# Kernel tuning notes

Hardware: AMD Instinct MI355X
Metric: run time of the kernel (lower is better)

The kernel has to match this reference:

```python
import jax, jax.numpy as jnp
import numpy as np

C = 192  # in_channels
B, S, L = 4, 64, 512  # batch, spatial (patch pixels), seq_len (num patches)


def setup_inputs() -> dict:
    key = jax.random.key(0)
    ks = jax.random.split(key, 6)
    scale_in = 1.0 / np.sqrt(C)
    return {
        "query": jax.random.normal(ks[0], (B, C, S, L), jnp.float32),
        "key": jax.random.normal(ks[1], (B, C, S, L), jnp.float32),
        "value": jax.random.normal(ks[2], (B, C, S, L), jnp.float32),
        "in_proj_weight": jax.random.normal(ks[3], (1 + 2 * C, C, 1, 1), jnp.float32) * scale_in,
        "in_proj_bias": jnp.zeros((1 + 2 * C,), jnp.float32),
        "out_proj_weight": jax.random.normal(ks[4], (C, C, 1, 1), jnp.float32) * scale_in,
        "out_proj_bias": jnp.zeros((C,), jnp.float32),
    }


def reference(query, key, value, in_proj_weight, in_proj_bias, out_proj_weight, out_proj_bias):
    # Separable (linear) attention, MobileViTv2-style.
    c = query.shape[1]
    w = in_proj_weight[:, :, 0, 0]           # (1+2C, C)
    wq, wk, wv = w[:1], w[1:1 + c], w[1 + c:]
    bq, bk, bv = in_proj_bias[:1], in_proj_bias[1:1 + c], in_proj_bias[1 + c:]

    # 1x1 conv projections (pointwise GEMMs over channels)
    q = jnp.einsum('oc,bcsl->bosl', wq, query) + bq[None, :, None, None]   # (B,1,S,L)
    k = jnp.einsum('oc,bcsl->bosl', wk, key) + bk[None, :, None, None]     # (B,C,S,L)
    v = jnp.einsum('oc,bcsl->bosl', wv, value) + bv[None, :, None, None]   # (B,C,S,L)

    # Context scores: softmax over token axis (seq_len); dropout_p=0 (eval)
    context_scores = jax.nn.softmax(q, axis=-1)                            # (B,1,S,L)

    # Weighted context pooling over tokens -> global context per spatial pixel
    context = jnp.sum(k * context_scores, axis=-1, keepdims=True)          # (B,C,S,1)

    # Broadcast multiply with gated value
    out = jax.nn.relu(v) * context                                         # (B,C,S,L)

    # Out projection (1x1 conv)
    wo = out_proj_weight[:, :, 0, 0]
    out = jnp.einsum('oc,bcsl->bosl', wo, out) + out_proj_bias[None, :, None, None]
    return out
```

## Files before the change

kernel.cpp:

```cpp
#include <hip/hip_runtime.h>

#define B_ 4
#define C_ 192
#define S_ 64
#define L_ 512

typedef _Float16 h8 __attribute__((ext_vector_type(8)));
typedef _Float16 h4 __attribute__((ext_vector_type(4)));
typedef _Float16 h2 __attribute__((ext_vector_type(2)));
typedef float f4 __attribute__((ext_vector_type(4)));

__device__ __forceinline__ int swz_l(int l) { return ((l >> 2) ^ l) & 7; }

__global__ __launch_bounds__(512) void k_prep(
    const float* __restrict__ W, const float* __restrict__ Bi,
    const float* __restrict__ Wo, const float* __restrict__ Bo,
    _Float16* __restrict__ wvh, _Float16* __restrict__ woh,
    float* __restrict__ bvf, float* __restrict__ bof,
    float* __restrict__ wkT)
{
    int n = blockIdx.x * 512 + threadIdx.x;
    if (n < 36864)       wvh[n] = (_Float16)W[37056 + n];
    else if (n < 73728)  woh[n - 36864] = (_Float16)Wo[n - 36864];
    else if (n < 73920)  bvf[n - 73728] = Bi[1 + C_ + (n - 73728)];
    else if (n < 74112)  bof[n - 73920] = Bo[n - 73920];
    else if (n < 110976) {
        int m = n - 74112;
        int c = m / C_, o = m - c * C_;
        wkT[m] = W[(1 + o) * C_ + c];
    }
}

__global__ __launch_bounds__(1024) void kA_front(
    const float* __restrict__ Q, const float* __restrict__ K,
    const float* __restrict__ W, const float* __restrict__ Bi,
    const float* __restrict__ wkT, float* __restrict__ ctxb)
{
    __shared__ __attribute__((aligned(16))) float sm_part[8 * 512];
    __shared__ float sm_p[512];
    __shared__ float sm_kbar[C_];
    __shared__ float sm_red[8];
    __shared__ float sm_red2[8];

    const int t = threadIdx.x;
    const int b = blockIdx.x >> 6, s = blockIdx.x & 63;
    const int lane = t & 63, w = t >> 6;

    {
        const int qid = t & 127;
        const int cg  = t >> 7;
        const float* qp = Q + (((size_t)b * C_ + cg * 24) * S_ + s) * L_ + qid * 4;
        f4 a; a[0] = 0.f; a[1] = 0.f; a[2] = 0.f; a[3] = 0.f;
#pragma unroll 8
        for (int c = 0; c < 24; ++c) {
            float wq = W[cg * 24 + c];
            f4 x = *(const f4*)(qp + (size_t)c * (S_ * L_));
            a[0] += wq * x[0]; a[1] += wq * x[1]; a[2] += wq * x[2]; a[3] += wq * x[3];
        }
        *(f4*)&sm_part[cg * 512 + qid * 4] = a;
    }
    __syncthreads();

    float q = 0.f, e = 0.f;
    if (t < 512) {
        q = ((sm_part[t] + sm_part[512 + t]) + (sm_part[1024 + t] + sm_part[1536 + t]))
          + ((sm_part[2048 + t] + sm_part[2560 + t]) + (sm_part[3072 + t] + sm_part[3584 + t]));
        float m = q;
#pragma unroll
        for (int off = 32; off >= 1; off >>= 1) m = fmaxf(m, __shfl_down(m, off));
        if (lane == 0) sm_red[w] = m;
    }
    __syncthreads();
    if (t < 512) {
        float bm = sm_red[0];
#pragma unroll
        for (int i = 1; i < 8; ++i) bm = fmaxf(bm, sm_red[i]);
        e = __expf(q - bm);
        float sum = e;
#pragma unroll
        for (int off = 32; off >= 1; off >>= 1) sum += __shfl_down(sum, off);
        if (lane == 0) sm_red2[w] = sum;
    }
    __syncthreads();
    if (t < 512) {
        float tot = 0.f;
#pragma unroll
        for (int i = 0; i < 8; ++i) tot += sm_red2[i];
        sm_p[t] = e / tot;
    }
    __syncthreads();

    {
        const f4* pp = (const f4*)sm_p;
        f4 p0 = pp[lane], p1 = pp[lane + 64];
#pragma unroll 4
        for (int r = 0; r < 12; ++r) {
            int c = w * 12 + r;
            const f4* kp = (const f4*)(K + (((size_t)b * C_ + c) * S_ + s) * L_);
            f4 x0 = kp[lane], x1 = kp[lane + 64];
            float d = x0[0]*p0[0] + x0[1]*p0[1] + x0[2]*p0[2] + x0[3]*p0[3]
                    + x1[0]*p1[0] + x1[1]*p1[1] + x1[2]*p1[2] + x1[3]*p1[3];
#pragma unroll
            for (int off = 32; off >= 1; off >>= 1) d += __shfl_down(d, off);
            if (lane == 0) sm_kbar[c] = d;
        }
    }
    __syncthreads();

    if (t < C_) {
        float a0 = 0.f, a1 = 0.f, a2 = 0.f, a3 = 0.f;
        for (int c = 0; c < C_; c += 4) {
            a0 += wkT[(c + 0) * C_ + t] * sm_kbar[c + 0];
            a1 += wkT[(c + 1) * C_ + t] * sm_kbar[c + 1];
            a2 += wkT[(c + 2) * C_ + t] * sm_kbar[c + 2];
            a3 += wkT[(c + 3) * C_ + t] * sm_kbar[c + 3];
        }
        ctxb[(size_t)blockIdx.x * C_ + t] = (a0 + a1) + (a2 + a3) + Bi[1 + t];
    }
}

__global__ __launch_bounds__(512, 4) void k_main(
    const float* __restrict__ V,
    const _Float16* __restrict__ wvh,
    const _Float16* __restrict__ woh,
    const float* __restrict__ ctxb,
    const float* __restrict__ bvf,
    const float* __restrict__ bof,
    float* __restrict__ Out)
{
    __shared__ __attribute__((aligned(16))) _Float16 sm_v[64 * 192];
    __shared__ __attribute__((aligned(16))) _Float16 sm_u[64 * 192];

    const int t = threadIdx.x;
    const int bs = blockIdx.x >> 3;
    const int chunk = blockIdx.x & 7;
    const int b = bs >> 6, s = bs & 63;
    const int l0 = chunk * 64;
    const int w = t >> 6, lane = t & 63;
    const int quad = lane >> 4, n16 = lane & 15;

    const int oB = (w & 3) * 48;
    const int lB = (w >> 2) * 32;

    {
        const int tx = t & 15, rp = t >> 4;
        h2* smv2 = (h2*)sm_v;
#pragma unroll
        for (int i = 0; i < 3; ++i) {
            int cp = i * 32 + rp;
            const float* vp = V + ((size_t)(b * C_ + 2 * cp) * S_ + s) * L_ + l0 + tx * 4;
            f4 x0 = *(const f4*)vp;
            f4 x1 = *(const f4*)(vp + S_ * L_);
#pragma unroll
            for (int k = 0; k < 4; ++k) {
                int l = tx * 4 + k;
                int dw = l * 96 + (((cp >> 2) ^ swz_l(l)) << 2) + (cp & 3);
                h2 hh; hh[0] = (_Float16)x0[k]; hh[1] = (_Float16)x1[k];
                smv2[dw] = hh;
            }
        }
    }

    h8 wv_fr[6][3];
#pragma unroll
    for (int kt = 0; kt < 6; ++kt)
#pragma unroll
        for (int i = 0; i < 3; ++i)
            wv_fr[kt][i] = *(const h8*)(wvh + (size_t)(oB + i * 16 + n16) * C_ + kt * 32 + quad * 8);

    __syncthreads();

    f4 acc[3][2];
#pragma unroll
    for (int i = 0; i < 3; ++i)
#pragma unroll
        for (int j = 0; j < 2; ++j) acc[i][j] = (f4)0.f;

#pragma unroll
    for (int kt = 0; kt < 6; ++kt) {
        h8 bfr[2];
#pragma unroll
        for (int j = 0; j < 2; ++j) {
            int l = lB + j * 16 + n16;
            bfr[j] = *(const h8*)(sm_v + l * 192 + (((kt * 4 + quad) ^ swz_l(l)) << 3));
        }
#pragma unroll
        for (int i = 0; i < 3; ++i)
#pragma unroll
            for (int j = 0; j < 2; ++j)
                acc[i][j] = __builtin_amdgcn_mfma_f32_16x16x32_f16(wv_fr[kt][i], bfr[j], acc[i][j], 0, 0, 0);
    }

    h8 wo_fr[6][3];
#pragma unroll
    for (int kt = 0; kt < 6; ++kt)
#pragma unroll
        for (int j = 0; j < 3; ++j)
            wo_fr[kt][j] = *(const h8*)(woh + (size_t)(oB + j * 16 + n16) * C_ + kt * 32 + quad * 8);

#pragma unroll
    for (int i = 0; i < 3; ++i) {
        int o0 = oB + i * 16 + quad * 4;
        f4 cx = *(const f4*)(ctxb + (size_t)bs * C_ + o0);
        f4 bv = *(const f4*)(bvf + o0);
#pragma unroll
        for (int j = 0; j < 2; ++j) {
            int l = lB + j * 16 + n16;
            h4 uu;
#pragma unroll
            for (int r = 0; r < 4; ++r) {
                float v = acc[i][j][r] + bv[r];
                uu[r] = (_Float16)(fmaxf(v, 0.f) * cx[r]);
            }
            *(h4*)(sm_u + l * 192 + (((o0 >> 3) ^ swz_l(l)) << 3) + (o0 & 7)) = uu;
        }
    }
    __syncthreads();

    f4 acc2[2][3];
#pragma unroll
    for (int i = 0; i < 2; ++i)
#pragma unroll
        for (int j = 0; j < 3; ++j) acc2[i][j] = (f4)0.f;

#pragma unroll
    for (int kt = 0; kt < 6; ++kt) {
        h8 afr2[2];
#pragma unroll
        for (int i = 0; i < 2; ++i) {
            int l = lB + i * 16 + n16;
            afr2[i] = *(const h8*)(sm_u + l * 192 + (((kt * 4 + quad) ^ swz_l(l)) << 3));
        }
#pragma unroll
        for (int j = 0; j < 3; ++j)
#pragma unroll
            for (int i = 0; i < 2; ++i)
                acc2[i][j] = __builtin_amdgcn_mfma_f32_16x16x32_f16(afr2[i], wo_fr[kt][j], acc2[i][j], 0, 0, 0);
    }

#pragma unroll
    for (int j = 0; j < 3; ++j) {
        int p = oB + j * 16 + n16;
        float bo = bof[p];
        float* obase = Out + ((size_t)(b * C_ + p) * S_ + s) * L_ + l0;
#pragma unroll
        for (int i = 0; i < 2; ++i) {
            int l = lB + i * 16 + quad * 4;
            f4 ov = acc2[i][j];
            ov[0] += bo; ov[1] += bo; ov[2] += bo; ov[3] += bo;
            *(f4*)(obase + l) = ov;
        }
    }
}

extern "C" void kernel_launch(void* const* d_in, const int* in_sizes, int n_in,
                              void* d_out, int out_size, void* d_ws, size_t ws_size,
                              hipStream_t stream) {
    const float* Q  = (const float*)d_in[0];
    const float* K  = (const float*)d_in[1];
    const float* V  = (const float*)d_in[2];
    const float* W  = (const float*)d_in[3];
    const float* Bi = (const float*)d_in[4];
    const float* Wo = (const float*)d_in[5];
    const float* Bo = (const float*)d_in[6];
    float* Out = (float*)d_out;

    char* ws = (char*)d_ws;
    _Float16* wvh = (_Float16*)(ws);
    _Float16* woh = (_Float16*)(ws + 73728);
    float*    bvf = (float*)(ws + 147456);
    float*    bof = (float*)(ws + 148224);
    float*    wkT = (float*)(ws + 148992);
    float*    ctxb = (float*)(ws + 296448);

    k_prep  <<<dim3(217),      dim3(512),  0, stream>>>(W, Bi, Wo, Bo, wvh, woh, bvf, bof, wkT);
    kA_front<<<dim3(B_ * S_),  dim3(1024), 0, stream>>>(Q, K, W, Bi, wkT, ctxb);
    k_main  <<<dim3(B_*S_*8),  dim3(512),  0, stream>>>(V, wvh, woh, ctxb, bvf, bof, Out);
}
```

Before: 372.8 us.

## Stage projection weights in LDS and double the L tile per block

The main kernel now runs 1024-thread blocks that each cover 128 sequence positions instead of 64, halving the grid. The Wv and Wo fp16 weights are no longer held as per-wave register fragments loaded from global memory. Instead they are staged cooperatively into a padded LDS buffer, Wv first and then Wo after the first GEMM, and read per k-step. Per-channel bias and context loads are hoisted ahead of the first GEMM. This cuts register pressure and redundant global weight fetches, but LDS use grows to about 126 KB per block, which limits a CU to one block and adds extra barriers plus a serial Wo staging step between the two GEMMs.

```diff
diff --git a/kernel.cpp b/kernel.cpp
--- a/kernel.cpp
+++ b/kernel.cpp
@@ -119,7 +119,7 @@
     }
 }
 
-__global__ __launch_bounds__(512, 4) void k_main(
+__global__ __launch_bounds__(1024, 4) void k_main(
     const float* __restrict__ V,
     const _Float16* __restrict__ wvh,
     const _Float16* __restrict__ woh,
@@ -128,23 +128,32 @@
     const float* __restrict__ bof,
     float* __restrict__ Out)
 {
-    __shared__ __attribute__((aligned(16))) _Float16 sm_v[64 * 192];
-    __shared__ __attribute__((aligned(16))) _Float16 sm_u[64 * 192];
+    __shared__ __attribute__((aligned(16))) _Float16 wbuf[192 * 200];
+    __shared__ __attribute__((aligned(16))) _Float16 vbuf[128 * 192];
 
     const int t = threadIdx.x;
-    const int bs = blockIdx.x >> 3;
-    const int chunk = blockIdx.x & 7;
+    const int bs = blockIdx.x >> 2;
+    const int chunk = blockIdx.x & 3;
     const int b = bs >> 6, s = bs & 63;
-    const int l0 = chunk * 64;
+    const int l0 = chunk * 128;
     const int w = t >> 6, lane = t & 63;
     const int quad = lane >> 4, n16 = lane & 15;
 
     const int oB = (w & 3) * 48;
     const int lB = (w >> 2) * 32;
 
+#pragma unroll
+    for (int i = 0; i < 5; ++i) {
+        int u = t + i * 1024;
+        if (u < 4608) {
+            int r = u / 24, c16 = u - r * 24;
+            *(f4*)(wbuf + r * 200 + c16 * 8) = *(const f4*)(wvh + r * 192 + c16 * 8);
+        }
+    }
+
     {
-        const int tx = t & 15, rp = t >> 4;
-        h2* smv2 = (h2*)sm_v;
+        const int tx = t & 31, rp = t >> 5;
+        h2* smv2 = (h2*)vbuf;
 #pragma unroll
         for (int i = 0; i < 3; ++i) {
             int cp = i * 32 + rp;
@@ -161,58 +170,64 @@
         }
     }
 
-    h8 wv_fr[6][3];
-#pragma unroll
-    for (int kt = 0; kt < 6; ++kt)
+    f4 cx[3], bvv[3];
+    float bo_r[3];
+#pragma unroll
+    for (int i = 0; i < 3; ++i) {
+        int o0 = oB + i * 16 + quad * 4;
+        cx[i]  = *(const f4*)(ctxb + (size_t)bs * C_ + o0);
+        bvv[i] = *(const f4*)(bvf + o0);
+        bo_r[i] = bof[oB + i * 16 + n16];
+    }
+    __syncthreads();
+
+    f4 acc[3][2];
+#pragma unroll
+    for (int i = 0; i < 3; ++i)
+#pragma unroll
+        for (int j = 0; j < 2; ++j) acc[i][j] = (f4)0.f;
+
+#pragma unroll
+    for (int kt = 0; kt < 6; ++kt) {
+        h8 afr[3];
 #pragma unroll
         for (int i = 0; i < 3; ++i)
-            wv_fr[kt][i] = *(const h8*)(wvh + (size_t)(oB + i * 16 + n16) * C_ + kt * 32 + quad * 8);
-
-    __syncthreads();
-
-    f4 acc[3][2];
-#pragma unroll
-    for (int i = 0; i < 3; ++i)
-#pragma unroll
-        for (int j = 0; j < 2; ++j) acc[i][j] = (f4)0.f;
-
-#pragma unroll
-    for (int kt = 0; kt < 6; ++kt) {
+            afr[i] = *(const h8*)(wbuf + (oB + i * 16 + n16) * 200 + kt * 32 + quad * 8);
         h8 bfr[2];
 #pragma unroll
         for (int j = 0; j < 2; ++j) {
             int l = lB + j * 16 + n16;
-            bfr[j] = *(const h8*)(sm_v + l * 192 + (((kt * 4 + quad) ^ swz_l(l)) << 3));
+            bfr[j] = *(const h8*)(vbuf + l * 192 + (((kt * 4 + quad) ^ swz_l(l)) << 3));
         }
 #pragma unroll
         for (int i = 0; i < 3; ++i)
 #pragma unroll
             for (int j = 0; j < 2; ++j)
-                acc[i][j] = __builtin_amdgcn_mfma_f32_16x16x32_f16(wv_fr[kt][i], bfr[j], acc[i][j], 0, 0, 0);
-    }
-
-    h8 wo_fr[6][3];
-#pragma unroll
-    for (int kt = 0; kt < 6; ++kt)
-#pragma unroll
-        for (int j = 0; j < 3; ++j)
-            wo_fr[kt][j] = *(const h8*)(woh + (size_t)(oB + j * 16 + n16) * C_ + kt * 32 + quad * 8);
-
+                acc[i][j] = __builtin_amdgcn_mfma_f32_16x16x32_f16(afr[i], bfr[j], acc[i][j], 0, 0, 0);
+    }
+    __syncthreads();
+
+#pragma unroll
+    for (int i = 0; i < 5; ++i) {
+        int u = t + i * 1024;
+        if (u < 4608) {
+            int r = u / 24, c16 = u - r * 24;
+            *(f4*)(wbuf + r * 200 + c16 * 8) = *(const f4*)(woh + r * 192 + c16 * 8);
+        }
+    }
 #pragma unroll
     for (int i = 0; i < 3; ++i) {
         int o0 = oB + i * 16 + quad * 4;
-        f4 cx = *(const f4*)(ctxb + (size_t)bs * C_ + o0);
-        f4 bv = *(const f4*)(bvf + o0);
 #pragma unroll
         for (int j = 0; j < 2; ++j) {
             int l = lB + j * 16 + n16;
             h4 uu;
 #pragma unroll
             for (int r = 0; r < 4; ++r) {
-                float v = acc[i][j][r] + bv[r];
-                uu[r] = (_Float16)(fmaxf(v, 0.f) * cx[r]);
+                float v = acc[i][j][r] + bvv[i][r];
+                uu[r] = (_Float16)(fmaxf(v, 0.f) * cx[i][r]);
             }
-            *(h4*)(sm_u + l * 192 + (((o0 >> 3) ^ swz_l(l)) << 3) + (o0 & 7)) = uu;
+            *(h4*)(vbuf + l * 192 + (((o0 >> 3) ^ swz_l(l)) << 3) + (o0 & 7)) = uu;
         }
     }
     __syncthreads();
@@ -229,19 +244,23 @@
 #pragma unroll
         for (int i = 0; i < 2; ++i) {
             int l = lB + i * 16 + n16;
-            afr2[i] = *(const h8*)(sm_u + l * 192 + (((kt * 4 + quad) ^ swz_l(l)) << 3));
-        }
+            afr2[i] = *(const h8*)(vbuf + l * 192 + (((kt * 4 + quad) ^ swz_l(l)) << 3));
+        }
+        h8 bfr2[3];
 #pragma unroll
         for (int j = 0; j < 3; ++j)
+            bfr2[j] = *(const h8*)(wbuf + (oB + j * 16 + n16) * 200 + kt * 32 + quad * 8);
+#pragma unroll
+        for (int j = 0; j < 3; ++j)
 #pragma unroll
             for (int i = 0; i < 2; ++i)
-                acc2[i][j] = __builtin_amdgcn_mfma_f32_16x16x32_f16(afr2[i], wo_fr[kt][j], acc2[i][j], 0, 0, 0);
+                acc2[i][j] = __builtin_amdgcn_mfma_f32_16x16x32_f16(afr2[i], bfr2[j], acc2[i][j], 0, 0, 0);
     }
 
 #pragma unroll
     for (int j = 0; j < 3; ++j) {
         int p = oB + j * 16 + n16;
-        float bo = bof[p];
+        float bo = bo_r[j];
         float* obase = Out + ((size_t)(b * C_ + p) * S_ + s) * L_ + l0;
 #pragma unroll
         for (int i = 0; i < 2; ++i) {
@@ -275,5 +294,5 @@
 
     k_prep  <<<dim3(217),      dim3(512),  0, stream>>>(W, Bi, Wo, Bo, wvh, woh, bvf, bof, wkT);
     kA_front<<<dim3(B_ * S_),  dim3(1024), 0, stream>>>(Q, K, W, Bi, wkT, ctxb);
-    k_main  <<<dim3(B_*S_*8),  dim3(512),  0, stream>>>(V, wvh, woh, ctxb, bvf, bof, Out);
-}
+    k_main  <<<dim3(B_*S_*4),  dim3(1024), 0, stream>>>(V, wvh, woh, ctxb, bvf, bof, Out);
+}
```

New measurement: 340.9 us. 1.09x faster.
